# Kernel tuning notes

Measured on AMD Instinct MI355X. Metric: run time of the kernel, lower is better.

## Reference

```python
import jax, jax.numpy as jnp
import numpy as np

N_SUPPORT = 8192
N_QUERY = 8192
INPUT_DIM = 1024
EMBED_DIM = 512
N_CLASSES = 64


def setup_inputs() -> dict:
    key = jax.random.key(0)
    k1, k2, k3, k4 = jax.random.split(key, 4)
    support_data = jax.random.normal(k1, (N_SUPPORT, INPUT_DIM), dtype=jnp.float32)
    query_data = jax.random.normal(k2, (N_QUERY, INPUT_DIM), dtype=jnp.float32)
    support_labels = jax.random.randint(k3, (N_SUPPORT,), 0, N_CLASSES, dtype=jnp.int32)
    W = jax.random.normal(k4, (INPUT_DIM, EMBED_DIM), dtype=jnp.float32) * (1.0 / np.sqrt(INPUT_DIM))
    return {"support_data": support_data, "support_labels": support_labels,
            "query_data": query_data, "W": W}


def _l2_normalize(x, eps=1e-12):
    # Matches F.normalize(p=2): x / max(||x||, eps)
    n = jnp.linalg.norm(x, axis=-1, keepdims=True)
    return x / jnp.maximum(n, eps)


def reference(support_data, support_labels, query_data, W):
    # encoder: single linear projection
    s_emb = support_data @ W            # [Ns, D]
    q_emb = query_data @ W              # [Nq, D]
    s_norm = _l2_normalize(s_emb)
    q_norm = _l2_normalize(q_emb)
    # cosine similarities for all query/support pairs: [Nq, Ns]
    sims = q_norm @ s_norm.T
    # per-class sum over support samples (torch.unique -> sorted 0..N_CLASSES-1)
    # segment_sum along the support axis: [N_classes, Nq] -> [Nq, N_classes]
    class_scores = jax.ops.segment_sum(sims.T, support_labels, num_segments=N_CLASSES).T
    return jax.nn.softmax(class_scores, axis=-1)
```

## Files before the change

kernel.cpp:

```cpp
#include <hip/hip_runtime.h>
#include <hip/hip_bf16.h>

#define NS 8192
#define NQ 8192
#define NTOT 16384
#define KDIM 1024
#define ED 512
#define NC 64
#define PBLK 64

typedef __attribute__((ext_vector_type(4))) float fx4;
typedef __attribute__((ext_vector_type(4))) int ix4;
typedef __attribute__((ext_vector_type(8))) short sx8;
typedef __attribute__((ext_vector_type(4))) unsigned short ux4;
typedef __attribute__((ext_vector_type(8))) unsigned short ux8;

__device__ __forceinline__ unsigned short f2bf(float f) {
  union { float f; unsigned u; } v; v.f = f;
  unsigned r = v.u + 0x7fffu + ((v.u >> 16) & 1u);
  return (unsigned short)(r >> 16);
}
__device__ __forceinline__ float bf2f(unsigned short h) {
  union { unsigned u; float f; } v; v.u = ((unsigned)h) << 16;
  return v.f;
}

__device__ __forceinline__ void async_ld16(const void* g, void* l) {
  __builtin_amdgcn_global_load_lds(
      (const __attribute__((address_space(1))) unsigned int*)g,
      (__attribute__((address_space(3))) unsigned int*)l, 16, 0, 0);
}

__global__ __launch_bounds__(256) void k_prep(
    const float* __restrict__ W, const float* __restrict__ Xs,
    const float* __restrict__ Xq, unsigned short* __restrict__ Wt,
    unsigned short* __restrict__ Xbf, float* __restrict__ rowssq) {
  __shared__ float tile[32][33];
  int bid = blockIdx.x;
  int t = threadIdx.x;
  if (bid < 512) {
    int k0 = (bid & 31) * 32;
    int n0 = (bid >> 5) * 32;
    int tx = t & 31, ty = t >> 5;
#pragma unroll
    for (int i = ty; i < 32; i += 8)
      tile[i][tx] = W[(size_t)(k0 + i) * ED + n0 + tx];
    __syncthreads();
#pragma unroll
    for (int i = ty; i < 32; i += 8)
      Wt[(size_t)(n0 + i) * KDIM + k0 + tx] = f2bf(tile[tx][i]);
  } else {
    int cb = bid - 512;
    const float* X = (cb < 1024) ? Xs : Xq;
    size_t src0 = (size_t)(cb & 1023) * 8192;
    size_t dst0 = (size_t)cb * 8192;
#pragma unroll
    for (int c = 0; c < 4; ++c) {
      size_t e = src0 + (size_t)c * 2048 + (size_t)t * 8;
      fx4 v0 = *(const fx4*)&X[e];
      fx4 v1 = *(const fx4*)&X[e + 4];
      ux8 b;
      b[0] = f2bf(v0.x); b[1] = f2bf(v0.y); b[2] = f2bf(v0.z); b[3] = f2bf(v0.w);
      b[4] = f2bf(v1.x); b[5] = f2bf(v1.y); b[6] = f2bf(v1.z); b[7] = f2bf(v1.w);
      *(ux8*)&Xbf[dst0 + (size_t)c * 2048 + (size_t)t * 8] = b;
    }
    if (cb < 8) {
#pragma unroll
      for (int i = t; i < 2048; i += 256) rowssq[cb * 2048 + i] = 0.f;
    }
  }
}

__global__ __launch_bounds__(256) void k_gemm_embed(
    const unsigned short* __restrict__ Xbf, const unsigned short* __restrict__ Wt,
    unsigned short* __restrict__ emb, float* __restrict__ rowssq) {
  __shared__ unsigned short Ash[2][128 * 8 * 8];
  __shared__ unsigned short Bsh[2][128 * 8 * 8];

  int lid = blockIdx.x;
  int x = lid & 7;
  int s = lid >> 3;
  int m_blk = x * 16 + (s >> 2);
  int n_blk = s & 3;

  const unsigned short* Xrow = Xbf + (size_t)m_blk * 128 * KDIM;
  const unsigned short* Wrow = Wt + (size_t)n_blk * 128 * KDIM;

  int t = threadIdx.x;
  int lane = t & 63, w = t >> 6;
  int wm = w >> 1, wn = w & 1;
  int quad = lane >> 4, ml = lane & 15;

  fx4 acc[4][4];
#pragma unroll
  for (int i = 0; i < 4; ++i)
#pragma unroll
    for (int j = 0; j < 4; ++j) acc[i][j] = fx4{0.f, 0.f, 0.f, 0.f};

  auto stage = [&](int kt, int b) {
    int k0 = kt * 64;
#pragma unroll
    for (int c = 0; c < 4; ++c) {
      int ch = t + 256 * c;
      int m = ch >> 3;
      int kq = (ch & 7) ^ (m & 7);
      async_ld16(&Xrow[(size_t)m * KDIM + k0 + kq * 8],
                 &Ash[b][(w * 64 + 256 * c) * 8]);
    }
#pragma unroll
    for (int c = 0; c < 4; ++c) {
      int ch = t + 256 * c;
      int n = ch >> 3;
      int kq = (ch & 7) ^ (n & 7);
      async_ld16(&Wrow[(size_t)n * KDIM + k0 + kq * 8],
                 &Bsh[b][(w * 64 + 256 * c) * 8]);
    }
  };

  stage(0, 0);
  for (int kt = 0; kt < 16; ++kt) {
    int b = kt & 1;
    __syncthreads();
    if (kt < 15) stage(kt + 1, b ^ 1);
#pragma unroll
    for (int s2 = 0; s2 < 2; ++s2) {
      int kq = s2 * 4 + quad;
      sx8 af[4], bfr[4];
#pragma unroll
      for (int i = 0; i < 4; ++i) {
        int row = wm * 64 + i * 16 + ml;
        af[i] = *(const sx8*)&Ash[b][(row * 8 + (kq ^ (row & 7))) * 8];
      }
#pragma unroll
      for (int j = 0; j < 4; ++j) {
        int nrow = wn * 64 + j * 16 + ml;
        bfr[j] = *(const sx8*)&Bsh[b][(nrow * 8 + (kq ^ (nrow & 7))) * 8];
      }
#pragma unroll
      for (int i = 0; i < 4; ++i)
#pragma unroll
        for (int j = 0; j < 4; ++j)
          acc[i][j] = __builtin_amdgcn_mfma_f32_16x16x32_bf16(af[i], bfr[j], acc[i][j], 0, 0, 0);
    }
  }

  int grow = m_blk * 128 + wm * 64;
  int gcol = n_blk * 128 + wn * 64;
#pragma unroll
  for (int i = 0; i < 4; ++i) {
#pragma unroll
    for (int r = 0; r < 4; ++r) {
      int mrow = grow + i * 16 + quad * 4 + r;
      float p = 0.f;
#pragma unroll
      for (int j = 0; j < 4; ++j) {
        emb[(size_t)mrow * ED + gcol + j * 16 + ml] = f2bf(acc[i][j][r]);
        p += acc[i][j][r] * acc[i][j][r];
      }
#pragma unroll
      for (int off = 1; off < 16; off <<= 1) p += __shfl_xor(p, off, 16);
      if (ml == 0) atomicAdd(&rowssq[mrow], p);
    }
  }
}

__global__ __launch_bounds__(256) void k_proto_partial(
    const unsigned short* __restrict__ embS, const float* __restrict__ rowssq,
    const int* __restrict__ labels, float* __restrict__ Ppart) {
  __shared__ float Pl[NC * 64];
  int t = threadIdx.x;
#pragma unroll
  for (int i = 0; i < 16; ++i) Pl[i * 256 + t] = 0.f;
  __syncthreads();

  int w = t >> 6, lane = t & 63;
  int ds = blockIdx.y;
  int row0 = blockIdx.x * (NS / PBLK);
#pragma unroll 4
  for (int r = w; r < NS / PBLK; r += 4) {
    int row = row0 + r;
    int lbl = labels[row];
    float scale = 1.0f / fmaxf(sqrtf(rowssq[row]), 1e-12f);
    float v = bf2f(embS[(size_t)row * ED + ds * 64 + lane]) * scale;
    atomicAdd(&Pl[lbl * 64 + lane], v);
  }
  __syncthreads();

  float* o = Ppart + (size_t)blockIdx.x * NC * ED + ds * 64;
#pragma unroll
  for (int i = 0; i < 16; ++i) {
    int idx = i * 256 + t;
    o[(size_t)(idx >> 6) * ED + (idx & 63)] = Pl[idx];
  }
}

__global__ __launch_bounds__(256) void k_proto_reduce(
    const float* __restrict__ Ppart, unsigned short* __restrict__ Pbf) {
  int idx = blockIdx.x * 256 + threadIdx.x;
  int kq = idx >> 9;
  int n = (idx >> 3) & 63;
  int j = idx & 7;
  int d = kq * 8 + j;
  float s = 0.f;
#pragma unroll 8
  for (int b = 0; b < PBLK; ++b) s += Ppart[(size_t)b * NC * ED + n * ED + d];
  Pbf[idx] = f2bf(s);
}

__global__ __launch_bounds__(64) void k_scores(
    const unsigned short* __restrict__ embQ, const float* __restrict__ ssqQ,
    const unsigned short* __restrict__ Pbf, float* __restrict__ out) {
  int lane = threadIdx.x;
  int quad = lane >> 4, ml = lane & 15;
  int qrow0 = blockIdx.x * 16;

  fx4 acc[4];
#pragma unroll
  for (int i = 0; i < 4; ++i) acc[i] = fx4{0.f, 0.f, 0.f, 0.f};

#pragma unroll 4
  for (int ki = 0; ki < 16; ++ki) {
    sx8 a = *(const sx8*)&embQ[(size_t)(qrow0 + ml) * ED + ki * 32 + quad * 8];
#pragma unroll
    for (int nt = 0; nt < 4; ++nt) {
      sx8 b = *(const sx8*)&Pbf[((ki * 4 + quad) * 64 + nt * 16 + ml) * 8];
      acc[nt] = __builtin_amdgcn_mfma_f32_16x16x32_bf16(a, b, acc[nt], 0, 0, 0);
    }
  }

#pragma unroll
  for (int r = 0; r < 4; ++r) {
    int qq = qrow0 + quad * 4 + r;
    float scale = 1.0f / fmaxf(sqrtf(ssqQ[qq]), 1e-12f);
    float s[4];
#pragma unroll
    for (int nt = 0; nt < 4; ++nt) s[nt] = acc[nt][r] * scale;
    float m = fmaxf(fmaxf(s[0], s[1]), fmaxf(s[2], s[3]));
#pragma unroll
    for (int off = 1; off < 16; off <<= 1) m = fmaxf(m, __shfl_xor(m, off, 16));
    float e[4], ssum = 0.f;
#pragma unroll
    for (int nt = 0; nt < 4; ++nt) { e[nt] = __expf(s[nt] - m); ssum += e[nt]; }
#pragma unroll
    for (int off = 1; off < 16; off <<= 1) ssum += __shfl_xor(ssum, off, 16);
    float inv = 1.0f / ssum;
#pragma unroll
    for (int nt = 0; nt < 4; ++nt)
      out[(size_t)qq * NC + nt * 16 + ml] = e[nt] * inv;
  }
}

extern "C" void kernel_launch(void* const* d_in, const int* in_sizes, int n_in,
                              void* d_out, int out_size, void* d_ws, size_t ws_size,
                              hipStream_t stream) {
  const float* Xs     = (const float*)d_in[0];
  const int*   labels = (const int*)d_in[1];
  const float* Xq     = (const float*)d_in[2];
  const float* W      = (const float*)d_in[3];
  float* out = (float*)d_out;

  char* ws = (char*)d_ws;
  size_t off = 0;
  unsigned short* Wt  = (unsigned short*)(ws + off); off += (size_t)ED * KDIM * 2;
  unsigned short* Xbf = (unsigned short*)(ws + off); off += (size_t)NTOT * KDIM * 2;
  unsigned short* emb = (unsigned short*)(ws + off); off += (size_t)NTOT * ED * 2;
  float* rowssq = (float*)(ws + off); off += (size_t)NTOT * 4;
  float* Ppart  = (float*)(ws + off); off += (size_t)PBLK * NC * ED * 4;
  unsigned short* Pbf = (unsigned short*)(ws + off); off += (size_t)NC * ED * 2;

  k_prep<<<2560, 256, 0, stream>>>(W, Xs, Xq, Wt, Xbf, rowssq);
  k_gemm_embed<<<512, 256, 0, stream>>>(Xbf, Wt, emb, rowssq);
  k_proto_partial<<<dim3(PBLK, 8), 256, 0, stream>>>(emb, rowssq, labels, Ppart);
  k_proto_reduce<<<NC * ED / 256, 256, 0, stream>>>(Ppart, Pbf);
  k_scores<<<NQ / 16, 64, 0, stream>>>(emb + (size_t)NS * ED, rowssq + NS, Pbf, out);
}
```

Baseline: 169.8 us.

## Fuse all stages into one cooperative persistent kernel with grid syncs

Replaces the five separate kernel launches (prep, embedding GEMM, prototype partial, prototype reduce, scoring) with a single cooperative kernel of 256 blocks that runs each stage in turn and separates them with grid-wide syncs. The aim is to remove launch gaps and inter-kernel drain/fill overhead. In exchange each stage runs with a fixed 256-block grid and one block per CU, which lowers parallelism and memory-level concurrency in the bandwidth-bound conversion and scoring stages. It also adds grid sync costs. The old multi-kernel path remains as a fallback if the cooperative launch fails.

```diff
diff --git a/kernel.cpp b/kernel.cpp
--- a/kernel.cpp
+++ b/kernel.cpp
@@ -1,5 +1,8 @@
 #include <hip/hip_runtime.h>
 #include <hip/hip_bf16.h>
+#include <hip/hip_cooperative_groups.h>
+
+namespace cg = cooperative_groups;
 
 #define NS 8192
 #define NQ 8192
@@ -12,7 +15,6 @@
 typedef __attribute__((ext_vector_type(4))) float fx4;
 typedef __attribute__((ext_vector_type(4))) int ix4;
 typedef __attribute__((ext_vector_type(8))) short sx8;
-typedef __attribute__((ext_vector_type(4))) unsigned short ux4;
 typedef __attribute__((ext_vector_type(8))) unsigned short ux8;
 
 __device__ __forceinline__ unsigned short f2bf(float f) {
@@ -29,6 +31,232 @@
   __builtin_amdgcn_global_load_lds(
       (const __attribute__((address_space(1))) unsigned int*)g,
       (__attribute__((address_space(3))) unsigned int*)l, 16, 0, 0);
+}
+
+union SM {
+  struct { unsigned short A[2][128 * 8 * 8]; unsigned short B[2][128 * 8 * 8]; } g;
+  float wtile[32][33];
+  float proto[NC * 128];
+};
+
+__global__ __launch_bounds__(256, 1) void k_fused(
+    const float* __restrict__ W, const float* __restrict__ Xs,
+    const float* __restrict__ Xq, const int* __restrict__ labels,
+    unsigned short* __restrict__ Wt, unsigned short* __restrict__ Xbf,
+    unsigned short* __restrict__ emb, float* __restrict__ rowssq,
+    float* __restrict__ Ppart, unsigned short* __restrict__ Pbf,
+    float* __restrict__ out) {
+  __shared__ SM sm;
+  cg::grid_group grid = cg::this_grid();
+
+  int lid = blockIdx.x;
+  int t = threadIdx.x;
+  int lane = t & 63, w = t >> 6;
+
+  {
+    const float* Xsrc = (lid < 128) ? Xs : Xq;
+    size_t src0 = (size_t)(lid & 127) * 65536;
+    size_t dst0 = (size_t)lid * 65536;
+#pragma unroll
+    for (int c = 0; c < 32; ++c) {
+      size_t e = src0 + (size_t)c * 2048 + (size_t)t * 8;
+      fx4 v0 = *(const fx4*)&Xsrc[e];
+      fx4 v1 = *(const fx4*)&Xsrc[e + 4];
+      ux8 b;
+      b[0] = f2bf(v0.x); b[1] = f2bf(v0.y); b[2] = f2bf(v0.z); b[3] = f2bf(v0.w);
+      b[4] = f2bf(v1.x); b[5] = f2bf(v1.y); b[6] = f2bf(v1.z); b[7] = f2bf(v1.w);
+      *(ux8*)&Xbf[dst0 + (size_t)c * 2048 + (size_t)t * 8] = b;
+    }
+    int tx = t & 31, ty = t >> 5;
+    for (int tt = lid; tt < 512; tt += 256) {
+      int k0 = (tt & 31) * 32;
+      int n0 = (tt >> 5) * 32;
+      __syncthreads();
+#pragma unroll
+      for (int i = ty; i < 32; i += 8)
+        sm.wtile[i][tx] = W[(size_t)(k0 + i) * ED + n0 + tx];
+      __syncthreads();
+#pragma unroll
+      for (int i = ty; i < 32; i += 8)
+        Wt[(size_t)(n0 + i) * KDIM + k0 + tx] = f2bf(sm.wtile[tx][i]);
+    }
+    if (t < 64) rowssq[lid * 64 + t] = 0.f;
+  }
+  grid.sync();
+
+  {
+    int wm = w >> 1, wn = w & 1;
+    int quad = lane >> 4, ml = lane & 15;
+
+    for (int tile = lid; tile < 512; tile += 256) {
+      int x = tile & 7;
+      int s = tile >> 3;
+      int m_blk = x * 16 + (s >> 2);
+      int n_blk = s & 3;
+
+      const unsigned short* Xrow = Xbf + (size_t)m_blk * 128 * KDIM;
+      const unsigned short* Wrow = Wt + (size_t)n_blk * 128 * KDIM;
+
+      fx4 acc[4][4];
+#pragma unroll
+      for (int i = 0; i < 4; ++i)
+#pragma unroll
+        for (int j = 0; j < 4; ++j) acc[i][j] = fx4{0.f, 0.f, 0.f, 0.f};
+
+      auto stage = [&](int kt, int b) {
+        int k0 = kt * 64;
+#pragma unroll
+        for (int c = 0; c < 4; ++c) {
+          int ch = t + 256 * c;
+          int m = ch >> 3;
+          int kq = (ch & 7) ^ (m & 7);
+          async_ld16(&Xrow[(size_t)m * KDIM + k0 + kq * 8],
+                     &sm.g.A[b][(w * 64 + 256 * c) * 8]);
+        }
+#pragma unroll
+        for (int c = 0; c < 4; ++c) {
+          int ch = t + 256 * c;
+          int n = ch >> 3;
+          int kq = (ch & 7) ^ (n & 7);
+          async_ld16(&Wrow[(size_t)n * KDIM + k0 + kq * 8],
+                     &sm.g.B[b][(w * 64 + 256 * c) * 8]);
+        }
+      };
+
+      stage(0, 0);
+      for (int kt = 0; kt < 16; ++kt) {
+        int b = kt & 1;
+        __syncthreads();
+        if (kt < 15) stage(kt + 1, b ^ 1);
+#pragma unroll
+        for (int s2 = 0; s2 < 2; ++s2) {
+          int kq = s2 * 4 + quad;
+          sx8 af[4], bfr[4];
+#pragma unroll
+          for (int i = 0; i < 4; ++i) {
+            int row = wm * 64 + i * 16 + ml;
+            af[i] = *(const sx8*)&sm.g.A[b][(row * 8 + (kq ^ (row & 7))) * 8];
+          }
+#pragma unroll
+          for (int j = 0; j < 4; ++j) {
+            int nrow = wn * 64 + j * 16 + ml;
+            bfr[j] = *(const sx8*)&sm.g.B[b][(nrow * 8 + (kq ^ (nrow & 7))) * 8];
+          }
+#pragma unroll
+          for (int i = 0; i < 4; ++i)
+#pragma unroll
+            for (int j = 0; j < 4; ++j)
+              acc[i][j] = __builtin_amdgcn_mfma_f32_16x16x32_bf16(af[i], bfr[j], acc[i][j], 0, 0, 0);
+        }
+      }
+
+      int grow = m_blk * 128 + wm * 64;
+      int gcol = n_blk * 128 + wn * 64;
+#pragma unroll
+      for (int i = 0; i < 4; ++i) {
+#pragma unroll
+        for (int r = 0; r < 4; ++r) {
+          int mrow = grow + i * 16 + quad * 4 + r;
+          float p = 0.f;
+#pragma unroll
+          for (int j = 0; j < 4; ++j) {
+            emb[(size_t)mrow * ED + gcol + j * 16 + ml] = f2bf(acc[i][j][r]);
+            p += acc[i][j][r] * acc[i][j][r];
+          }
+#pragma unroll
+          for (int off = 1; off < 16; off <<= 1) p += __shfl_xor(p, off, 16);
+          if (ml == 0) atomicAdd(&rowssq[mrow], p);
+        }
+      }
+      __syncthreads();
+    }
+  }
+  grid.sync();
+
+  {
+    int chunk = lid & 63;
+    int ds = lid >> 6;
+#pragma unroll
+    for (int i = 0; i < 32; ++i) sm.proto[i * 256 + t] = 0.f;
+    __syncthreads();
+
+    int row0 = chunk * 128;
+#pragma unroll 4
+    for (int r = w; r < 128; r += 4) {
+      int row = row0 + r;
+      int lbl = labels[row];
+      float scale = 1.0f / fmaxf(sqrtf(rowssq[row]), 1e-12f);
+      const unsigned short* er = &emb[(size_t)row * ED + ds * 128];
+      float v0 = bf2f(er[lane]) * scale;
+      float v1 = bf2f(er[lane + 64]) * scale;
+      atomicAdd(&sm.proto[lbl * 128 + lane], v0);
+      atomicAdd(&sm.proto[lbl * 128 + lane + 64], v1);
+    }
+    __syncthreads();
+
+    float* o = Ppart + (size_t)chunk * NC * ED + ds * 128;
+#pragma unroll
+    for (int i = 0; i < 32; ++i) {
+      int idx = i * 256 + t;
+      o[(size_t)(idx >> 7) * ED + (idx & 127)] = sm.proto[idx];
+    }
+  }
+  grid.sync();
+
+  if (lid < 128) {
+    int idx = lid * 256 + t;
+    int kq = idx >> 9;
+    int n = (idx >> 3) & 63;
+    int j = idx & 7;
+    int d = kq * 8 + j;
+    float s = 0.f;
+#pragma unroll 8
+    for (int b = 0; b < 64; ++b) s += Ppart[(size_t)b * NC * ED + n * ED + d];
+    Pbf[idx] = f2bf(s);
+  }
+  grid.sync();
+
+  if (w < 2) {
+    int quad = lane >> 4, ml = lane & 15;
+    int qrow0 = lid * 32 + w * 16;
+    const unsigned short* embQ = emb + (size_t)NS * ED;
+    const float* ssqQ = rowssq + NS;
+
+    fx4 acc[4];
+#pragma unroll
+    for (int i = 0; i < 4; ++i) acc[i] = fx4{0.f, 0.f, 0.f, 0.f};
+
+#pragma unroll 4
+    for (int ki = 0; ki < 16; ++ki) {
+      sx8 a = *(const sx8*)&embQ[(size_t)(qrow0 + ml) * ED + ki * 32 + quad * 8];
+#pragma unroll
+      for (int nt = 0; nt < 4; ++nt) {
+        sx8 b = *(const sx8*)&Pbf[((ki * 4 + quad) * 64 + nt * 16 + ml) * 8];
+        acc[nt] = __builtin_amdgcn_mfma_f32_16x16x32_bf16(a, b, acc[nt], 0, 0, 0);
+      }
+    }
+
+#pragma unroll
+    for (int r = 0; r < 4; ++r) {
+      int qq = qrow0 + quad * 4 + r;
+      float scale = 1.0f / fmaxf(sqrtf(ssqQ[qq]), 1e-12f);
+      float s[4];
+#pragma unroll
+      for (int nt = 0; nt < 4; ++nt) s[nt] = acc[nt][r] * scale;
+      float m = fmaxf(fmaxf(s[0], s[1]), fmaxf(s[2], s[3]));
+#pragma unroll
+      for (int off = 1; off < 16; off <<= 1) m = fmaxf(m, __shfl_xor(m, off, 16));
+      float e[4], ssum = 0.f;
+#pragma unroll
+      for (int nt = 0; nt < 4; ++nt) { e[nt] = __expf(s[nt] - m); ssum += e[nt]; }
+#pragma unroll
+      for (int off = 1; off < 16; off <<= 1) ssum += __shfl_xor(ssum, off, 16);
+      float inv = 1.0f / ssum;
+#pragma unroll
+      for (int nt = 0; nt < 4; ++nt)
+        out[(size_t)qq * NC + nt * 16 + ml] = e[nt] * inv;
+    }
+  }
 }
 
 __global__ __launch_bounds__(256) void k_prep(
@@ -268,9 +496,17 @@
   float* Ppart  = (float*)(ws + off); off += (size_t)PBLK * NC * ED * 4;
   unsigned short* Pbf = (unsigned short*)(ws + off); off += (size_t)NC * ED * 2;
 
-  k_prep<<<2560, 256, 0, stream>>>(W, Xs, Xq, Wt, Xbf, rowssq);
-  k_gemm_embed<<<512, 256, 0, stream>>>(Xbf, Wt, emb, rowssq);
-  k_proto_partial<<<dim3(PBLK, 8), 256, 0, stream>>>(emb, rowssq, labels, Ppart);
-  k_proto_reduce<<<NC * ED / 256, 256, 0, stream>>>(Ppart, Pbf);
-  k_scores<<<NQ / 16, 64, 0, stream>>>(emb + (size_t)NS * ED, rowssq + NS, Pbf, out);
-}
+  void* args[] = {(void*)&W, (void*)&Xs, (void*)&Xq, (void*)&labels,
+                  (void*)&Wt, (void*)&Xbf, (void*)&emb, (void*)&rowssq,
+                  (void*)&Ppart, (void*)&Pbf, (void*)&out};
+  hipError_t err = hipLaunchCooperativeKernel((const void*)k_fused, dim3(256),
+                                              dim3(256), args, 0, stream);
+  if (err != hipSuccess) {
+    (void)hipGetLastError();
+    k_prep<<<2560, 256, 0, stream>>>(W, Xs, Xq, Wt, Xbf, rowssq);
+    k_gemm_embed<<<512, 256, 0, stream>>>(Xbf, Wt, emb, rowssq);
+    k_proto_partial<<<dim3(PBLK, 8), 256, 0, stream>>>(emb, rowssq, labels, Ppart);
+    k_proto_reduce<<<NC * ED / 256, 256, 0, stream>>>(Ppart, Pbf);
+    k_scores<<<NQ / 16, 64, 0, stream>>>(emb + (size_t)NS * ED, rowssq + NS, Pbf, out);
+  }
+}
```

Measured after the change: 337.1 us. 98.5% more time.

## Fuse prototype accumulation, reduction and scoring into one cooperative kernel

Applied to the files above, without the earlier changes.

Replaces the three tail kernels (per-class partial sums, partial reduction, query scoring with softmax) with a single cooperative kernel of 256 blocks that uses grid-wide syncs between phases. The aim is to remove two kernel-launch gaps and their drain/fill time at the end of the pipeline. In exchange, each phase runs on only 256 blocks, so partial sums use 32 chunks instead of 64 and scoring uses two waves per block. Grid syncs add their own latency. A fallback to the old three-kernel path runs if the cooperative launch fails.

```diff
diff --git a/kernel.cpp b/kernel.cpp
--- a/kernel.cpp
+++ b/kernel.cpp
@@ -1,5 +1,8 @@
 #include <hip/hip_runtime.h>
 #include <hip/hip_bf16.h>
+#include <hip/hip_cooperative_groups.h>
+
+namespace cg = cooperative_groups;
 
 #define NS 8192
 #define NQ 8192
@@ -12,7 +15,6 @@
 typedef __attribute__((ext_vector_type(4))) float fx4;
 typedef __attribute__((ext_vector_type(4))) int ix4;
 typedef __attribute__((ext_vector_type(8))) short sx8;
-typedef __attribute__((ext_vector_type(4))) unsigned short ux4;
 typedef __attribute__((ext_vector_type(8))) unsigned short ux8;
 
 __device__ __forceinline__ unsigned short f2bf(float f) {
@@ -164,6 +166,95 @@
   }
 }
 
+__global__ __launch_bounds__(256, 1) void k_tail(
+    const unsigned short* __restrict__ emb, const float* __restrict__ rowssq,
+    const int* __restrict__ labels, float* __restrict__ Ppart,
+    unsigned short* __restrict__ Pbf, float* __restrict__ out) {
+  __shared__ float Pl[NC * 64];
+  cg::grid_group grid = cg::this_grid();
+  int lid = blockIdx.x, t = threadIdx.x;
+  int lane = t & 63, w = t >> 6;
+
+  {
+    int chunk = lid >> 3, ds = lid & 7;
+#pragma unroll
+    for (int i = 0; i < 16; ++i) Pl[i * 256 + t] = 0.f;
+    __syncthreads();
+    int row0 = chunk * 256;
+#pragma unroll 4
+    for (int r = w; r < 256; r += 4) {
+      int row = row0 + r;
+      int lbl = labels[row];
+      float scale = 1.0f / fmaxf(sqrtf(rowssq[row]), 1e-12f);
+      float v = bf2f(emb[(size_t)row * ED + ds * 64 + lane]) * scale;
+      atomicAdd(&Pl[lbl * 64 + lane], v);
+    }
+    __syncthreads();
+    float* o = Ppart + (size_t)chunk * NC * ED + ds * 64;
+#pragma unroll
+    for (int i = 0; i < 16; ++i) {
+      int idx = i * 256 + t;
+      o[(size_t)(idx >> 6) * ED + (idx & 63)] = Pl[idx];
+    }
+  }
+  grid.sync();
+
+  if (lid < 128) {
+    int idx = lid * 256 + t;
+    int kq = idx >> 9;
+    int n = (idx >> 3) & 63;
+    int j = idx & 7;
+    int d = kq * 8 + j;
+    float s = 0.f;
+#pragma unroll 8
+    for (int b = 0; b < 32; ++b) s += Ppart[(size_t)b * NC * ED + n * ED + d];
+    Pbf[idx] = f2bf(s);
+  }
+  grid.sync();
+
+  if (w < 2) {
+    int quad = lane >> 4, ml = lane & 15;
+    int qrow0 = lid * 32 + w * 16;
+    const unsigned short* embQ = emb + (size_t)NS * ED;
+    const float* ssqQ = rowssq + NS;
+
+    fx4 acc[4];
+#pragma unroll
+    for (int i = 0; i < 4; ++i) acc[i] = fx4{0.f, 0.f, 0.f, 0.f};
+
+#pragma unroll 4
+    for (int ki = 0; ki < 16; ++ki) {
+      sx8 a = *(const sx8*)&embQ[(size_t)(qrow0 + ml) * ED + ki * 32 + quad * 8];
+#pragma unroll
+      for (int nt = 0; nt < 4; ++nt) {
+        sx8 b = *(const sx8*)&Pbf[((ki * 4 + quad) * 64 + nt * 16 + ml) * 8];
+        acc[nt] = __builtin_amdgcn_mfma_f32_16x16x32_bf16(a, b, acc[nt], 0, 0, 0);
+      }
+    }
+
+#pragma unroll
+    for (int r = 0; r < 4; ++r) {
+      int qq = qrow0 + quad * 4 + r;
+      float scale = 1.0f / fmaxf(sqrtf(ssqQ[qq]), 1e-12f);
+      float s[4];
+#pragma unroll
+      for (int nt = 0; nt < 4; ++nt) s[nt] = acc[nt][r] * scale;
+      float m = fmaxf(fmaxf(s[0], s[1]), fmaxf(s[2], s[3]));
+#pragma unroll
+      for (int off = 1; off < 16; off <<= 1) m = fmaxf(m, __shfl_xor(m, off, 16));
+      float e[4], ssum = 0.f;
+#pragma unroll
+      for (int nt = 0; nt < 4; ++nt) { e[nt] = __expf(s[nt] - m); ssum += e[nt]; }
+#pragma unroll
+      for (int off = 1; off < 16; off <<= 1) ssum += __shfl_xor(ssum, off, 16);
+      float inv = 1.0f / ssum;
+#pragma unroll
+      for (int nt = 0; nt < 4; ++nt)
+        out[(size_t)qq * NC + nt * 16 + ml] = e[nt] * inv;
+    }
+  }
+}
+
 __global__ __launch_bounds__(256) void k_proto_partial(
     const unsigned short* __restrict__ embS, const float* __restrict__ rowssq,
     const int* __restrict__ labels, float* __restrict__ Ppart) {
@@ -270,7 +361,16 @@
 
   k_prep<<<2560, 256, 0, stream>>>(W, Xs, Xq, Wt, Xbf, rowssq);
   k_gemm_embed<<<512, 256, 0, stream>>>(Xbf, Wt, emb, rowssq);
-  k_proto_partial<<<dim3(PBLK, 8), 256, 0, stream>>>(emb, rowssq, labels, Ppart);
-  k_proto_reduce<<<NC * ED / 256, 256, 0, stream>>>(Ppart, Pbf);
-  k_scores<<<NQ / 16, 64, 0, stream>>>(emb + (size_t)NS * ED, rowssq + NS, Pbf, out);
-}
+
+  const unsigned short* embC = emb;
+  void* args[] = {(void*)&embC, (void*)&rowssq, (void*)&labels,
+                  (void*)&Ppart, (void*)&Pbf, (void*)&out};
+  hipError_t err = hipLaunchCooperativeKernel((const void*)k_tail, dim3(256),
+                                              dim3(256), args, 0, stream);
+  if (err != hipSuccess) {
+    (void)hipGetLastError();
+    k_proto_partial<<<dim3(PBLK, 8), 256, 0, stream>>>(emb, rowssq, labels, Ppart);
+    k_proto_reduce<<<NC * ED / 256, 256, 0, stream>>>(Ppart, Pbf);
+    k_scores<<<NQ / 16, 64, 0, stream>>>(emb + (size_t)NS * ED, rowssq + NS, Pbf, out);
+  }
+}
```

New measurement: 244.5 us. 44.0% more time.
